# Kernel tuning notes

Measured on AMD Instinct MI355X. Metric: run time of the kernel, lower is better.

## Reference

```python
import jax, jax.numpy as jnp
import numpy as np

B = 1024          # batch
IN_FEATURES = 20000
N_GROUP = 64
G_IN = 512        # indices gathered per group
H1 = 256          # first Linear out dim per group
GROUP_SIZE = 128  # second Linear out dim per group


def setup_inputs() -> dict:
    key = jax.random.key(0)
    k_x, k_idx, k_w1, k_b1, k_w2, k_b2 = jax.random.split(key, 6)
    x = jax.random.normal(k_x, (B, IN_FEATURES), dtype=jnp.float32)
    idx = jax.random.randint(k_idx, (N_GROUP, G_IN), 0, IN_FEATURES, dtype=jnp.int64)
    # Stacked per-group Linear weights (uniform group shapes allow batching).
    s1 = 1.0 / np.sqrt(G_IN)
    s2 = 1.0 / np.sqrt(H1)
    W1 = jax.random.uniform(k_w1, (N_GROUP, G_IN, H1), jnp.float32, -s1, s1)
    b1 = jax.random.uniform(k_b1, (N_GROUP, H1), jnp.float32, -s1, s1)
    W2 = jax.random.uniform(k_w2, (N_GROUP, H1, GROUP_SIZE), jnp.float32, -s2, s2)
    b2 = jax.random.uniform(k_b2, (N_GROUP, GROUP_SIZE), jnp.float32, -s2, s2)
    return {"x": x, "idx": idx, "W1": W1, "b1": b1, "W2": W2, "b2": b2}


def reference(x, idx, W1, b1, W2, b2):
    # Per-group gather of input columns: [B, n_group, G_IN]
    g = x[:, idx]
    # Two bare Linears per group (no activation, matching the source Sequential).
    h = jnp.einsum('bgi,gio->bgo', g, W1) + b1          # [B, n_group, H1]
    o = jnp.einsum('bgh,gho->bgo', h, W2) + b2          # [B, n_group, GROUP_SIZE]
    # Concat groups along feature dim -> [B, n_group*GROUP_SIZE]
    return o.reshape(o.shape[0], -1)
```

## Files before the change

kernel.cpp:

```cpp
#include <hip/hip_runtime.h>
#include <hip/hip_bf16.h>
#include <stdint.h>


typedef __attribute__((ext_vector_type(4))) float f32x4;
typedef __attribute__((ext_vector_type(8))) __bf16 bf16x8;
typedef __attribute__((ext_vector_type(8))) uint16_t u16x8;

__device__ __forceinline__ uint16_t f2bf(float f) {
    uint32_t u = __float_as_uint(f);
    u += 0x7FFFu + ((u >> 16) & 1u);
    return (uint16_t)(u >> 16);
}

__device__ __forceinline__ uint64_t pack4bf(f32x4 v) {
    return (uint64_t)f2bf(v[0]) | ((uint64_t)f2bf(v[1]) << 16)
         | ((uint64_t)f2bf(v[2]) << 32) | ((uint64_t)f2bf(v[3]) << 48);
}

__device__ __forceinline__ void row_load(const float* __restrict__ xrow, int t, f32x4 r[5]) {
    #pragma unroll
    for (int i = 0; i < 5; ++i) {
        int si = t + i * 1024;
        si = si < 4999 ? si : 4999;
        r[i] = *(const f32x4*)(xrow + (size_t)si * 4);
    }
}

__device__ __forceinline__ void row_write(uint16_t* sh, int t, const f32x4 r[5]) {
    #pragma unroll
    for (int i = 0; i < 5; ++i) {
        int si = t + i * 1024;
        if (si < 5000) *(uint64_t*)&sh[si * 4] = pack4bf(r[i]);
    }
}

__device__ __forceinline__ void row_gather(const uint16_t* sh, const int4* __restrict__ idx4,
                                           int t, int b, uint32_t* __restrict__ G32) {
    int4 nv = idx4[t];
    #pragma unroll
    for (int it = 0; it < 8; ++it) {
        int4 cv = nv;
        if (it < 7) nv = idx4[t + (it + 1) * 1024];
        int j = t + it * 1024;
        uint32_t w0 = (uint32_t)sh[cv.x] | ((uint32_t)sh[cv.y] << 16);
        uint32_t w1 = (uint32_t)sh[cv.z] | ((uint32_t)sh[cv.w] << 16);
        int g = j >> 7, kd = j & 127;
        uint2 p; p.x = w0; p.y = w1;
        *(uint2*)&G32[(size_t)g * 262144 + (size_t)b * 256 + kd * 2] = p;
    }
}

__global__ __launch_bounds__(1024, 8) void k_prep(const float* __restrict__ x,
                                                  const int* __restrict__ idx,
                                                  const float* __restrict__ W1,
                                                  const float* __restrict__ b1,
                                                  const float* __restrict__ W2,
                                                  const float* __restrict__ b2,
                                                  uint16_t* __restrict__ Wc,
                                                  float* __restrict__ bias2,
                                                  uint32_t* __restrict__ G32) {
    __shared__ __align__(16) uint8_t smem[40960];
    const int bid = blockIdx.x;
    const int t = threadIdx.x;

    if (bid < 256) {
        uint16_t* As = (uint16_t*)smem;
        uint16_t* Bs = As + 5120;
        const int g = bid >> 2, mt = bid & 3;
        const int wid = t >> 6, l = t & 63;
        const int wm = wid >> 2, wn = wid & 3;
        const int q = l >> 4, lm = l & 15;
        const float* W1g = W1 + ((size_t)g * 512 + (size_t)mt * 128) * 256;
        const float* W2g = W2 + (size_t)g * 256 * 128;
        f32x4 acc[2][2];
        #pragma unroll
        for (int mi = 0; mi < 2; ++mi)
            #pragma unroll
            for (int ni = 0; ni < 2; ++ni) {
                f32x4 z = {0.f, 0.f, 0.f, 0.f};
                acc[mi][ni] = z;
            }
        for (int kt = 0; kt < 8; ++kt) {
            __syncthreads();
            {
                int m = t >> 3, c4 = t & 7;
                f32x4 v = *(const f32x4*)(W1g + (size_t)m * 256 + kt * 32 + c4 * 4);
                *(uint64_t*)&As[m * 40 + c4 * 4] = pack4bf(v);
            }
            {
                int h = t >> 5, n4 = t & 31;
                f32x4 v = *(const f32x4*)(W2g + (size_t)(kt * 32 + h) * 128 + n4 * 4);
                *(uint64_t*)&Bs[h * 132 + n4 * 4] = pack4bf(v);
            }
            __syncthreads();
            bf16x8 a[2];
            #pragma unroll
            for (int mi = 0; mi < 2; ++mi)
                a[mi] = *(const bf16x8*)&As[(wm * 32 + mi * 16 + lm) * 40 + q * 8];
            #pragma unroll
            for (int ni = 0; ni < 2; ++ni) {
                int n = wn * 32 + ni * 16 + lm;
                u16x8 bu;
                #pragma unroll
                for (int j = 0; j < 8; ++j) bu[j] = Bs[(q * 8 + j) * 132 + n];
                bf16x8 bv = __builtin_bit_cast(bf16x8, bu);
                #pragma unroll
                for (int mi = 0; mi < 2; ++mi)
                    acc[mi][ni] = __builtin_amdgcn_mfma_f32_16x16x32_bf16(a[mi], bv, acc[mi][ni], 0, 0, 0);
            }
        }
        uint16_t* Wcg = Wc + (size_t)g * 128 * 512;
        #pragma unroll
        for (int mi = 0; mi < 2; ++mi) {
            int k0 = mt * 128 + wm * 32 + mi * 16 + q * 4;
            #pragma unroll
            for (int ni = 0; ni < 2; ++ni) {
                int n = wn * 32 + ni * 16 + lm;
                *(uint64_t*)&Wcg[(size_t)n * 512 + k0] = pack4bf(acc[mi][ni]);
            }
        }
    } else if (bid < 320) {
        if (t < 128) {
            const int g = bid - 256, n = t;
            const float* w = W2 + (size_t)g * 256 * 128 + n;
            const float* bb = b1 + g * 256;
            float s = b2[g * 128 + n];
            for (int h = 0; h < 256; ++h) s += bb[h] * w[(size_t)h * 128];
            bias2[g * 128 + n] = s;
        }
    } else {
        uint16_t* sh = (uint16_t*)smem;
        const int gb = bid - 320;
        const int b0 = gb * 2, b1r = b0 + 1;
        const int4* idx4 = (const int4*)idx;
        f32x4 r[5];
        row_load(x + (size_t)b0 * 20000, t, r);
        row_write(sh, t, r);
        __syncthreads();
        row_load(x + (size_t)b1r * 20000, t, r);
        __builtin_amdgcn_sched_barrier(0);
        row_gather(sh, idx4, t, b0, G32);
        __syncthreads();
        row_write(sh, t, r);
        __syncthreads();
        row_gather(sh, idx4, t, b1r, G32);
    }
}

__global__ __launch_bounds__(256) void k_gemm(const uint16_t* __restrict__ G,
                                              const uint16_t* __restrict__ Wc,
                                              const float* __restrict__ bias2,
                                              float* __restrict__ out) {
    __shared__ uint16_t sh[16384];
    uint16_t* As = sh;
    uint16_t* Bs = sh + 8192;
    const int wg = (blockIdx.x & 7) * 64 + (blockIdx.x >> 3);
    const int g = wg >> 3, mt = wg & 7;
    const int t = threadIdx.x;
    const int wid = t >> 6, l = t & 63;
    const int wm = wid >> 1, wn = wid & 1;
    const int q = l >> 4, lm = l & 15;
    const int lrow = l >> 3;
    const int lcolsw = ((l & 7) ^ lrow) * 8;
    const uint16_t* Ga = G + (size_t)g * 524288 + (size_t)mt * 128 * 512;
    const uint16_t* Wa = Wc + (size_t)g * 65536;

    f32x4 acc[4][4];
    #pragma unroll
    for (int mi = 0; mi < 4; ++mi)
        #pragma unroll
        for (int ni = 0; ni < 4; ++ni) {
            f32x4 z = {0.f, 0.f, 0.f, 0.f};
            acc[mi][ni] = z;
        }

    for (int kt = 0; kt < 8; ++kt) {
        __syncthreads();
        #pragma unroll
        for (int r = 0; r < 4; ++r) {
            const int rowbase = wid * 8 + r * 32;
            const uint16_t* sA = Ga + (size_t)(rowbase + lrow) * 512 + kt * 64 + lcolsw;
            const uint16_t* sB = Wa + (size_t)(rowbase + lrow) * 512 + kt * 64 + lcolsw;
            __builtin_amdgcn_global_load_lds(
                (const __attribute__((address_space(1))) void*)sA,
                (__attribute__((address_space(3))) void*)(As + rowbase * 64), 16, 0, 0);
            __builtin_amdgcn_global_load_lds(
                (const __attribute__((address_space(1))) void*)sB,
                (__attribute__((address_space(3))) void*)(Bs + rowbase * 64), 16, 0, 0);
        }
        __syncthreads();
        #pragma unroll
        for (int kk = 0; kk < 2; ++kk) {
            bf16x8 a[4], b[4];
            #pragma unroll
            for (int mi = 0; mi < 4; ++mi) {
                int row = wm * 64 + mi * 16 + lm;
                int off = row * 64 + ((kk * 32 + q * 8) ^ ((lm & 7) * 8));
                a[mi] = *(const bf16x8*)&As[off];
            }
            #pragma unroll
            for (int ni = 0; ni < 4; ++ni) {
                int row = wn * 64 + ni * 16 + lm;
                int off = row * 64 + ((kk * 32 + q * 8) ^ ((lm & 7) * 8));
                b[ni] = *(const bf16x8*)&Bs[off];
            }
            #pragma unroll
            for (int mi = 0; mi < 4; ++mi)
                #pragma unroll
                for (int ni = 0; ni < 4; ++ni)
                    acc[mi][ni] = __builtin_amdgcn_mfma_f32_16x16x32_bf16(a[mi], b[ni], acc[mi][ni], 0, 0, 0);
        }
    }
    float bn[4];
    #pragma unroll
    for (int ni = 0; ni < 4; ++ni) bn[ni] = bias2[g * 128 + wn * 64 + ni * 16 + lm];
    #pragma unroll
    for (int mi = 0; mi < 4; ++mi)
        #pragma unroll
        for (int ni = 0; ni < 4; ++ni) {
            int col = g * 128 + wn * 64 + ni * 16 + lm;
            #pragma unroll
            for (int r = 0; r < 4; ++r) {
                int brow = mt * 128 + wm * 64 + mi * 16 + q * 4 + r;
                out[(size_t)brow * 8192 + col] = acc[mi][ni][r] + bn[ni];
            }
        }
}

extern "C" void kernel_launch(void* const* d_in, const int* in_sizes, int n_in,
                              void* d_out, int out_size, void* d_ws, size_t ws_size,
                              hipStream_t stream) {
    (void)in_sizes; (void)n_in; (void)out_size; (void)ws_size;
    const float* x   = (const float*)d_in[0];
    const int*   idx = (const int*)d_in[1];
    const float* W1  = (const float*)d_in[2];
    const float* b1  = (const float*)d_in[3];
    const float* W2  = (const float*)d_in[4];
    const float* b2  = (const float*)d_in[5];
    float* out = (float*)d_out;

    uint16_t* G     = (uint16_t*)d_ws;
    uint16_t* Wc    = (uint16_t*)((char*)d_ws + (size_t)(64 << 20));
    float*    bias2 = (float*)   ((char*)d_ws + (size_t)(72 << 20));

    k_prep<<<832, 1024, 0, stream>>>(x, idx, W1, b1, W2, b2, Wc, bias2, (uint32_t*)G);
    k_gemm<<<512,  256, 0, stream>>>(G, Wc, bias2, out);
}
```

Baseline: 69.29 us.

## Stage x rows into LDS via direct global-to-LDS loads, one row per block

The gather path now loads each x row as fp32 straight into LDS with global_load_lds and converts to bf16 only for the gathered elements, using the packed v_cvt_pk_bf16_f32 instruction. Each block handles one batch row instead of two, so the grid grows from 832 to 1344 blocks. This removes the register round-trip and the bf16 packing of the whole row. In exchange the LDS footprint doubles to 80KB per block, which lowers occupancy, and the two-row overlap of loading and gathering is gone.

After: 58.31 us. -15.8%, faster.

```diff
diff --git a/kernel.cpp b/kernel.cpp
--- a/kernel.cpp
+++ b/kernel.cpp
@@ -16,39 +16,6 @@
 __device__ __forceinline__ uint64_t pack4bf(f32x4 v) {
     return (uint64_t)f2bf(v[0]) | ((uint64_t)f2bf(v[1]) << 16)
          | ((uint64_t)f2bf(v[2]) << 32) | ((uint64_t)f2bf(v[3]) << 48);
-}
-
-__device__ __forceinline__ void row_load(const float* __restrict__ xrow, int t, f32x4 r[5]) {
-    #pragma unroll
-    for (int i = 0; i < 5; ++i) {
-        int si = t + i * 1024;
-        si = si < 4999 ? si : 4999;
-        r[i] = *(const f32x4*)(xrow + (size_t)si * 4);
-    }
-}
-
-__device__ __forceinline__ void row_write(uint16_t* sh, int t, const f32x4 r[5]) {
-    #pragma unroll
-    for (int i = 0; i < 5; ++i) {
-        int si = t + i * 1024;
-        if (si < 5000) *(uint64_t*)&sh[si * 4] = pack4bf(r[i]);
-    }
-}
-
-__device__ __forceinline__ void row_gather(const uint16_t* sh, const int4* __restrict__ idx4,
-                                           int t, int b, uint32_t* __restrict__ G32) {
-    int4 nv = idx4[t];
-    #pragma unroll
-    for (int it = 0; it < 8; ++it) {
-        int4 cv = nv;
-        if (it < 7) nv = idx4[t + (it + 1) * 1024];
-        int j = t + it * 1024;
-        uint32_t w0 = (uint32_t)sh[cv.x] | ((uint32_t)sh[cv.y] << 16);
-        uint32_t w1 = (uint32_t)sh[cv.z] | ((uint32_t)sh[cv.w] << 16);
-        int g = j >> 7, kd = j & 127;
-        uint2 p; p.x = w0; p.y = w1;
-        *(uint2*)&G32[(size_t)g * 262144 + (size_t)b * 256 + kd * 2] = p;
-    }
 }
 
 __global__ __launch_bounds__(1024, 8) void k_prep(const float* __restrict__ x,
@@ -60,7 +27,7 @@
                                                   uint16_t* __restrict__ Wc,
                                                   float* __restrict__ bias2,
                                                   uint32_t* __restrict__ G32) {
-    __shared__ __align__(16) uint8_t smem[40960];
+    __shared__ __align__(16) uint8_t smem[81920];
     const int bid = blockIdx.x;
     const int t = threadIdx.x;
 
@@ -130,21 +97,35 @@
             bias2[g * 128 + n] = s;
         }
     } else {
-        uint16_t* sh = (uint16_t*)smem;
-        const int gb = bid - 320;
-        const int b0 = gb * 2, b1r = b0 + 1;
+        float* shf = (float*)smem;
+        const int b = bid - 320;
+        const float* xrow = x + (size_t)b * 20000;
+        const int wb = (t >> 6) << 6;
+        #pragma unroll
+        for (int i = 0; i < 5; ++i) {
+            int c = t + i * 1024;
+            int csrc = c < 5000 ? c : 4999;
+            __builtin_amdgcn_global_load_lds(
+                (const __attribute__((address_space(1))) void*)(xrow + (size_t)csrc * 4),
+                (__attribute__((address_space(3))) void*)(shf + (size_t)(wb + i * 1024) * 4),
+                16, 0, 0);
+        }
+        __syncthreads();
         const int4* idx4 = (const int4*)idx;
-        f32x4 r[5];
-        row_load(x + (size_t)b0 * 20000, t, r);
-        row_write(sh, t, r);
-        __syncthreads();
-        row_load(x + (size_t)b1r * 20000, t, r);
-        __builtin_amdgcn_sched_barrier(0);
-        row_gather(sh, idx4, t, b0, G32);
-        __syncthreads();
-        row_write(sh, t, r);
-        __syncthreads();
-        row_gather(sh, idx4, t, b1r, G32);
+        int4 nv = idx4[t];
+        #pragma unroll
+        for (int it = 0; it < 8; ++it) {
+            int4 cv = nv;
+            if (it < 7) nv = idx4[t + (it + 1) * 1024];
+            float f0 = shf[cv.x], f1 = shf[cv.y], f2 = shf[cv.z], f3 = shf[cv.w];
+            uint32_t w0, w1;
+            asm("v_cvt_pk_bf16_f32 %0, %1, %2" : "=v"(w0) : "v"(f0), "v"(f1));
+            asm("v_cvt_pk_bf16_f32 %0, %1, %2" : "=v"(w1) : "v"(f2), "v"(f3));
+            int j = t + it * 1024;
+            int g = j >> 7, kd = j & 127;
+            uint2 p; p.x = w0; p.y = w1;
+            *(uint2*)&G32[(size_t)g * 262144 + (size_t)b * 256 + kd * 2] = p;
+        }
     }
 }
 
@@ -244,6 +225,6 @@
     uint16_t* Wc    = (uint16_t*)((char*)d_ws + (size_t)(64 << 20));
     float*    bias2 = (float*)   ((char*)d_ws + (size_t)(72 << 20));
 
-    k_prep<<<832, 1024, 0, stream>>>(x, idx, W1, b1, W2, b2, Wc, bias2, (uint32_t*)G);
+    k_prep<<<1344, 1024, 0, stream>>>(x, idx, W1, b1, W2, b2, Wc, bias2, (uint32_t*)G);
     k_gemm<<<512,  256, 0, stream>>>(G, Wc, bias2, out);
 }
```

## Double-buffer staged x rows, hoist packed indices, use hardware bf16 convert

Applied to the files above, without the earlier changes.

The gather path of the prep kernel now stages the two batch rows in separate LDS buffers. This removes the barrier that made the second row's write wait until the first row's gather had finished. The gather indices are loaded once up front and packed two per 32-bit register, so they are no longer reloaded for each row. The software float-to-bf16 rounding is replaced by the packed v_cvt_pk_bf16_f32 instruction. In exchange, LDS per block grows to 80 KB of dynamic shared memory for every block, and more registers stay live through the gather.

Measured after the change: 76.37 us. 10.2% more time.

```diff
diff --git a/kernel.cpp b/kernel.cpp
--- a/kernel.cpp
+++ b/kernel.cpp
@@ -18,36 +18,40 @@
          | ((uint64_t)f2bf(v[2]) << 32) | ((uint64_t)f2bf(v[3]) << 48);
 }
 
-__device__ __forceinline__ void row_load(const float* __restrict__ xrow, int t, f32x4 r[5]) {
+__device__ __forceinline__ void stage_row(uint16_t* buf, int t, const f32x4 r[5]) {
     #pragma unroll
     for (int i = 0; i < 5; ++i) {
-        int si = t + i * 1024;
-        si = si < 4999 ? si : 4999;
-        r[i] = *(const f32x4*)(xrow + (size_t)si * 4);
-    }
-}
-
-__device__ __forceinline__ void row_write(uint16_t* sh, int t, const f32x4 r[5]) {
+        int c = t + i * 1024;
+        uint32_t lo, hi;
+        asm("v_cvt_pk_bf16_f32 %0, %1, %2" : "=v"(lo) : "v"(r[i][0]), "v"(r[i][1]));
+        asm("v_cvt_pk_bf16_f32 %0, %1, %2" : "=v"(hi) : "v"(r[i][2]), "v"(r[i][3]));
+        uint2 p2; p2.x = lo; p2.y = hi;
+        *(uint2*)&buf[c * 4] = p2;
+    }
+}
+
+__device__ __forceinline__ void load_row(const float* __restrict__ xrow, int t, f32x4 r[5]) {
     #pragma unroll
     for (int i = 0; i < 5; ++i) {
-        int si = t + i * 1024;
-        if (si < 5000) *(uint64_t*)&sh[si * 4] = pack4bf(r[i]);
-    }
-}
-
-__device__ __forceinline__ void row_gather(const uint16_t* sh, const int4* __restrict__ idx4,
+        int c = t + i * 1024;
+        int cs = c < 5000 ? c : 4999;
+        r[i] = *(const f32x4*)(xrow + (size_t)cs * 4);
+    }
+}
+
+__device__ __forceinline__ void gather_row(const uint16_t* buf, const uint32_t pk[16],
                                            int t, int b, uint32_t* __restrict__ G32) {
-    int4 nv = idx4[t];
     #pragma unroll
     for (int it = 0; it < 8; ++it) {
-        int4 cv = nv;
-        if (it < 7) nv = idx4[t + (it + 1) * 1024];
+        uint32_t pa = pk[2 * it], pb = pk[2 * it + 1];
+        uint32_t f0 = buf[pa & 0xffffu], f1 = buf[pa >> 16];
+        uint32_t f2 = buf[pb & 0xffffu], f3 = buf[pb >> 16];
+        uint2 p;
+        p.x = f0 | (f1 << 16);
+        p.y = f2 | (f3 << 16);
         int j = t + it * 1024;
-        uint32_t w0 = (uint32_t)sh[cv.x] | ((uint32_t)sh[cv.y] << 16);
-        uint32_t w1 = (uint32_t)sh[cv.z] | ((uint32_t)sh[cv.w] << 16);
-        int g = j >> 7, kd = j & 127;
-        uint2 p; p.x = w0; p.y = w1;
-        *(uint2*)&G32[(size_t)g * 262144 + (size_t)b * 256 + kd * 2] = p;
+        int g = j >> 7, kq = j & 127;
+        *(uint2*)&G32[(size_t)g * 262144 + (size_t)b * 256 + kq * 2] = p;
     }
 }
 
@@ -60,7 +64,7 @@
                                                   uint16_t* __restrict__ Wc,
                                                   float* __restrict__ bias2,
                                                   uint32_t* __restrict__ G32) {
-    __shared__ __align__(16) uint8_t smem[40960];
+    extern __shared__ __align__(16) uint8_t smem[];
     const int bid = blockIdx.x;
     const int t = threadIdx.x;
 
@@ -130,21 +134,34 @@
             bias2[g * 128 + n] = s;
         }
     } else {
-        uint16_t* sh = (uint16_t*)smem;
+        uint16_t* buf0 = (uint16_t*)smem;
+        uint16_t* buf1 = buf0 + 20480;
         const int gb = bid - 320;
-        const int b0 = gb * 2, b1r = b0 + 1;
+        const int b0 = gb * 2;
+        const float* xr0 = x + (size_t)b0 * 20000;
+        const float* xr1 = xr0 + 20000;
+
         const int4* idx4 = (const int4*)idx;
+        uint32_t pk[16];
+        #pragma unroll
+        for (int p = 0; p < 8; ++p) {
+            int4 iv = idx4[t + p * 1024];
+            pk[2 * p]     = (uint32_t)iv.x | ((uint32_t)iv.y << 16);
+            pk[2 * p + 1] = (uint32_t)iv.z | ((uint32_t)iv.w << 16);
+        }
+
         f32x4 r[5];
-        row_load(x + (size_t)b0 * 20000, t, r);
-        row_write(sh, t, r);
-        __syncthreads();
-        row_load(x + (size_t)b1r * 20000, t, r);
+        load_row(xr0, t, r);
+        stage_row(buf0, t, r);
+        __syncthreads();
+
+        load_row(xr1, t, r);
         __builtin_amdgcn_sched_barrier(0);
-        row_gather(sh, idx4, t, b0, G32);
-        __syncthreads();
-        row_write(sh, t, r);
-        __syncthreads();
-        row_gather(sh, idx4, t, b1r, G32);
+        gather_row(buf0, pk, t, b0, G32);
+        __builtin_amdgcn_sched_barrier(0);
+        stage_row(buf1, t, r);
+        __syncthreads();
+        gather_row(buf1, pk, t, b0 + 1, G32);
     }
 }
 
@@ -244,6 +261,6 @@
     uint16_t* Wc    = (uint16_t*)((char*)d_ws + (size_t)(64 << 20));
     float*    bias2 = (float*)   ((char*)d_ws + (size_t)(72 << 20));
 
-    k_prep<<<832, 1024, 0, stream>>>(x, idx, W1, b1, W2, b2, Wc, bias2, (uint32_t*)G);
+    k_prep<<<832, 1024, 81920, stream>>>(x, idx, W1, b1, W2, b2, Wc, bias2, (uint32_t*)G);
     k_gemm<<<512,  256, 0, stream>>>(G, Wc, bias2, out);
 }
```
